# Optimization experiments

Hardware: AMD Instinct MI355X
Metric: run time of the kernel (lower is better)

## Reference

```python
import jax, jax.numpy as jnp
import numpy as np

N, F_IN, H, C, E = 50000, 512, 128, 64, 800000


def setup_inputs() -> dict:
    key = jax.random.key(0)
    ks = jax.random.split(key, 20)
    stdv = 1.0 / np.sqrt(H)
    std_att = 1.0
    std_att_vec = 1.0 / np.sqrt(3.0)
    u = lambda k, shape, s: jax.random.uniform(k, shape, jnp.float32, -s, s)
    inp = {
        "x": jax.random.normal(ks[0], (N, F_IN), jnp.float32),
        "edge_row": jax.random.randint(ks[1], (E,), 0, N, jnp.int32),
        "edge_col": jax.random.randint(ks[2], (E,), 0, N, jnp.int32),
        "edge_val": jax.random.uniform(ks[3], (E,), jnp.float32) * (1.0 / 16.0),
        "weight_low": u(ks[4], (F_IN, H), stdv),
        "weight_high": u(ks[5], (F_IN, H), stdv),
        "weight_mlp": u(ks[6], (F_IN, H), stdv),
        "att_vec_low": u(ks[7], (H, 1), std_att),
        "att_vec_high": u(ks[8], (H, 1), std_att),
        "att_vec_mlp": u(ks[9], (H, 1), std_att),
        "att_vec": u(ks[10], (3, 3), std_att_vec),
        "weight_low2": u(ks[11], (H, C), stdv),
        "weight_high2": u(ks[12], (H, C), stdv),
        "weight_mlp2": u(ks[13], (H, C), stdv),
        "att_vec_low2": u(ks[14], (C, 1), std_att),
        "att_vec_high2": u(ks[15], (C, 1), std_att),
        "att_vec_mlp2": u(ks[16], (C, 1), std_att),
        "att_vec2": u(ks[17], (3, 3), std_att_vec),
    }
    return inp


def _spmm_low(row, col, val, X):
    # adj_low @ X via gather + segment-sum over edges
    return jax.ops.segment_sum(val[:, None] * X[col], row, num_segments=N)


def _attention(o_low, o_high, o_mlp, a_low, a_high, a_mlp, a_vec):
    T = 3.0
    feats = jnp.concatenate([o_low @ a_low, o_high @ a_high, o_mlp @ a_mlp], axis=1)  # [N,3]
    att = jax.nn.softmax(jax.nn.sigmoid(feats) @ a_vec / T, axis=1)
    return att[:, 0:1], att[:, 1:2], att[:, 2:3]


def _layer(X, row, col, val, W_l, W_h, W_m, a_l, a_h, a_m, a_vec):
    xl = X @ W_l
    xh = X @ W_h
    o_low = jax.nn.relu(_spmm_low(row, col, val, xl))
    o_high = jax.nn.relu(xh - _spmm_low(row, col, val, xh))  # (I - adj_low) @ xh
    o_mlp = jax.nn.relu(X @ W_m)
    al, ah, am = _attention(o_low, o_high, o_mlp, a_l, a_h, a_m, a_vec)
    return 3.0 * (al * o_low + ah * o_high + am * o_mlp)


def reference(x, edge_row, edge_col, edge_val, weight_low, weight_high, weight_mlp,
              att_vec_low, att_vec_high, att_vec_mlp, att_vec,
              weight_low2, weight_high2, weight_mlp2,
              att_vec_low2, att_vec_high2, att_vec_mlp2, att_vec2):
    h = _layer(x, edge_row, edge_col, edge_val, weight_low, weight_high, weight_mlp,
               att_vec_low, att_vec_high, att_vec_mlp, att_vec)
    out = _layer(h, edge_row, edge_col, edge_val, weight_low2, weight_high2, weight_mlp2,
                 att_vec_low2, att_vec_high2, att_vec_mlp2, att_vec2)
    return jax.nn.log_softmax(out, axis=1)
```

## Files before the change

kernel.cpp:

```cpp
#include <hip/hip_runtime.h>
#include <hip/hip_bf16.h>

#define NN 50000
#define F_IN 512
#define HH 128
#define CC 64

typedef __attribute__((ext_vector_type(8))) short short8v;
typedef __attribute__((ext_vector_type(4))) float f32x4;
typedef __attribute__((ext_vector_type(2))) float f32x2;

__device__ __forceinline__ short f2b(float f) {
    unsigned u = __builtin_bit_cast(unsigned, f);
    unsigned r = (u + 0x7fffu + ((u >> 16) & 1u)) >> 16;
    return (short)r;
}
__device__ __forceinline__ float b2f(short s) {
    unsigned u = ((unsigned)(unsigned short)s) << 16;
    return __builtin_bit_cast(float, u);
}
__device__ __forceinline__ float b2f_lo(unsigned p) {
    return __builtin_bit_cast(float, p << 16);
}
__device__ __forceinline__ float b2f_hi(unsigned p) {
    return __builtin_bit_cast(float, p & 0xffff0000u);
}

__device__ __forceinline__ f32x2 q2_lo(unsigned p) {
    return __builtin_amdgcn_cvt_pk_f32_fp8(p, false);
}
__device__ __forceinline__ f32x2 q2_hi(unsigned p) {
    return __builtin_amdgcn_cvt_pk_f32_fp8(p, true);
}

__device__ __forceinline__ int xcd_swz(int bid, int nwg) {
    int q = nwg >> 3, r = nwg & 7;
    int xcd = bid & 7, off = bid >> 3;
    return (xcd < r ? xcd * (q + 1) : r * (q + 1) + (xcd - r) * q) + off;
}

__device__ __forceinline__ void load_lds16(const short* g, short* l) {
    __builtin_amdgcn_global_load_lds(
        (const __attribute__((address_space(1))) unsigned int*)g,
        (__attribute__((address_space(3))) unsigned int*)l,
        16, 0, 0);
}

template <int K, int OUTW>
__device__ __forceinline__ void wprep_body(const float* __restrict__ W0,
                                           const float* __restrict__ W1,
                                           const float* __restrict__ W2,
                                           short* __restrict__ Bt, int id) {
    const int nth = 3 * OUTW * (K / 8);
    if (id >= nth) return;
    const int n = id / (K / 8);
    const int kq = id % (K / 8);
    constexpr int HB = OUTW / 2;
    const int t = n / OUTW;
    const int r = n % OUTW;
    int sel, c;
    if (t < 2) { sel = (r >= HB) ? 1 : 0; c = t * HB + (r % HB); }
    else       { sel = 2; c = r; }
    const float* W = sel == 0 ? W0 : (sel == 1 ? W1 : W2);
    short v[8];
#pragma unroll
    for (int j = 0; j < 8; ++j) v[j] = f2b(W[(size_t)(kq * 8 + j) * OUTW + c]);
#pragma unroll
    for (int j = 0; j < 8; ++j) Bt[(size_t)n * K + kq * 8 + j] = v[j];
}

__global__ __launch_bounds__(256) void prep0(int* __restrict__ counts, int n,
                                             const float* __restrict__ Wl,
                                             const float* __restrict__ Wh,
                                             const float* __restrict__ Wm,
                                             short* __restrict__ Bt1,
                                             const float* __restrict__ Wl2,
                                             const float* __restrict__ Wh2,
                                             const float* __restrict__ Wm2,
                                             short* __restrict__ Bt2,
                                             int nZero, int nW1) {
    const int b = blockIdx.x;
    if (b < nZero) {
        int i = b * 256 + threadIdx.x;
        if (i < n) counts[i] = 0;
    } else if (b < nZero + nW1) {
        wprep_body<F_IN, HH>(Wl, Wh, Wm, Bt1, (b - nZero) * 256 + threadIdx.x);
    } else {
        wprep_body<HH, CC>(Wl2, Wh2, Wm2, Bt2, (b - nZero - nW1) * 256 + threadIdx.x);
    }
}

__global__ __launch_bounds__(256) void hist_xconv(const int* __restrict__ erow,
                                                  int* __restrict__ counts, int E,
                                                  const float* __restrict__ x,
                                                  short* __restrict__ xb, int n8,
                                                  int nHist) {
    const int b = blockIdx.x;
    const int total = gridDim.x;
    const long hb4 = ((long)b * nHist) / total;
    const long ha4 = ((long)(b + 1) * nHist) / total;
    if (ha4 != hb4) {
        int i = (int)hb4 * 256 + threadIdx.x;
        if (i < E) atomicAdd(&counts[erow[i]], 1);
        return;
    }
    int i = (b - (int)hb4) * 256 + threadIdx.x;
    if (i >= n8) return;
    const float4* xp = (const float4*)x;
    const float4 a = xp[2 * i];
    const float4 bb = xp[2 * i + 1];
    short8v o;
    o[0] = f2b(a.x); o[1] = f2b(a.y); o[2] = f2b(a.z); o[3] = f2b(a.w);
    o[4] = f2b(bb.x); o[5] = f2b(bb.y); o[6] = f2b(bb.z); o[7] = f2b(bb.w);
    *reinterpret_cast<short8v*>(&xb[(size_t)i * 8]) = o;
}

template <int K, int BNout>
__device__ __forceinline__ void gemm_body(const short* __restrict__ A,
                                          const short* __restrict__ Bt,
                                          unsigned* __restrict__ xq,
                                          short* __restrict__ xh,
                                          short* __restrict__ xm,
                                          int M, int wg, short* smem) {
    constexpr int BM = 128, BK = 64;
    constexpr int FM = (BNout == 128) ? 4 : 2;
    constexpr int FN = 4;
    constexpr int WM = FM * 16;
    constexpr int NKT = K / BK;
    constexpr int NBL = BNout / 32;
    constexpr int HB = BNout / 2;

    short* As = smem;
    short* Bs = smem + BM * BK;

    const int tid = threadIdx.x;
    const int lane = tid & 63;
    const int wid = tid >> 6;
    const int bm = wg / 3;
    const int bn = wg % 3;
    const int m0 = bm * BM;
    const int n0 = bn * BNout;
    const int wm = (BNout == 128) ? (wid >> 1) : wid;
    const int wn = (BNout == 128) ? (wid & 1) : 0;

    const int r8 = lane >> 3;
    const int sl = (lane & 7) ^ r8;

    f32x4 acc[FM][FN];
#pragma unroll
    for (int i = 0; i < FM; ++i)
#pragma unroll
        for (int j = 0; j < FN; ++j) acc[i][j] = (f32x4){0.f, 0.f, 0.f, 0.f};

    for (int kt = 0; kt < NKT; ++kt) {
        const int k0 = kt * BK;
        __syncthreads();
#pragma unroll
        for (int i = 0; i < 4; ++i) {
            int r = (wid * 4 + i) * 8 + r8;
            int gr = m0 + r; if (gr >= M) gr = M - 1;
            load_lds16(&A[(size_t)gr * K + k0 + sl * 8], &As[(wid * 4 + i) * 512]);
        }
#pragma unroll
        for (int i = 0; i < NBL; ++i) {
            int r = (wid * NBL + i) * 8 + r8;
            load_lds16(&Bt[(size_t)(n0 + r) * K + k0 + sl * 8],
                       &Bs[(wid * NBL + i) * 512]);
        }
        __syncthreads();

        const int mrow = lane & 15;
        const int kg = lane >> 4;
#pragma unroll
        for (int kk = 0; kk < 2; ++kk) {
            short8v af[FM], bf[FN];
#pragma unroll
            for (int f = 0; f < FM; ++f) {
                int m = wm * WM + f * 16 + mrow;
                int s = kk * 4 + kg;
                af[f] = *reinterpret_cast<const short8v*>(
                    &As[m * 64 + ((s ^ (m & 7)) << 3)]);
            }
#pragma unroll
            for (int f = 0; f < FN; ++f) {
                int nr = wn * 64 + f * 16 + mrow;
                int s = kk * 4 + kg;
                bf[f] = *reinterpret_cast<const short8v*>(
                    &Bs[nr * 64 + ((s ^ (nr & 7)) << 3)]);
            }
#pragma unroll
            for (int i = 0; i < FM; ++i)
#pragma unroll
                for (int j = 0; j < FN; ++j)
                    acc[i][j] = __builtin_amdgcn_mfma_f32_16x16x32_bf16(
                        af[i], bf[j], acc[i][j], 0, 0, 0);
        }
    }

    __syncthreads();
#pragma unroll
    for (int i = 0; i < FM; ++i)
#pragma unroll
        for (int j = 0; j < FN; ++j) {
            int cc = wn * 64 + j * 16 + (lane & 15);
#pragma unroll
            for (int e = 0; e < 4; ++e) {
                int r = wm * WM + i * 16 + (lane >> 4) * 4 + e;
                smem[r * BNout + cc] = f2b(acc[i][j][e]);
            }
        }
    __syncthreads();

    if (bn == 2) {
        constexpr int CH = BM * BNout / 8;
#pragma unroll
        for (int p = 0; p < CH / 256; ++p) {
            int idx = p * 256 + tid;
            int r = idx / (BNout / 8);
            int c8 = idx % (BNout / 8);
            int grow = m0 + r;
            if (grow < M)
                *reinterpret_cast<int4*>(&xm[(size_t)grow * BNout + c8 * 8]) =
                    *reinterpret_cast<const int4*>(&smem[r * BNout + c8 * 8]);
        }
    } else {
#pragma unroll
        for (int p = 0; p < (BM * (HB / 8)) / 256; ++p) {
            int idx = p * 256 + tid;
            int r = idx / (HB / 8);
            int c8 = idx % (HB / 8);
            int grow = m0 + r;
            if (grow < M)
                *reinterpret_cast<int4*>(&xh[(size_t)grow * BNout + bn * HB + c8 * 8]) =
                    *reinterpret_cast<const int4*>(&smem[r * BNout + HB + c8 * 8]);
        }
#pragma unroll
        for (int p = 0; p < (BM * (BNout / 4)) / 256; ++p) {
            int idx = p * 256 + tid;
            int r = idx / (BNout / 4);
            int k = idx % (BNout / 4);
            int grow = m0 + r;
            if (grow < M) {
                unsigned lw = *reinterpret_cast<const unsigned*>(&smem[r * BNout + 2 * k]);
                unsigned hw = *reinterpret_cast<const unsigned*>(&smem[r * BNout + HB + 2 * k]);
                unsigned w;
                if (BNout == 128) {
                    w = __builtin_amdgcn_cvt_pk_fp8_f32(b2f_lo(lw), b2f_hi(lw), 0, false);
                    w = __builtin_amdgcn_cvt_pk_fp8_f32(b2f_lo(hw), b2f_hi(hw), w, true);
                } else {
                    w = __builtin_amdgcn_cvt_pk_fp8_f32(b2f_lo(lw), b2f_lo(hw), 0, false);
                    w = __builtin_amdgcn_cvt_pk_fp8_f32(b2f_hi(lw), b2f_hi(hw), w, true);
                }
                xq[(size_t)grow * (BNout / 2) + bn * (BNout / 4) + k] = w;
            }
        }
    }
}

template <int K, int BNout>
__global__ __launch_bounds__(256) void gemm_scatter(const short* __restrict__ A,
                                                    const short* __restrict__ Bt,
                                                    unsigned* __restrict__ xq,
                                                    short* __restrict__ xh,
                                                    short* __restrict__ xm,
                                                    int M, int nGemm,
                                                    const int* __restrict__ row,
                                                    const int* __restrict__ col,
                                                    const float* __restrict__ val,
                                                    int* __restrict__ cursor,
                                                    int2* __restrict__ edges, int E,
                                                    int nScat) {
    __shared__ short smem[128 * 64 + BNout * 64];

    const int total = nGemm + nScat;
    const int swz = xcd_swz(blockIdx.x, total);
    const long ns_b = ((long)swz * nScat) / total;
    const long ns_a = ((long)(swz + 1) * nScat) / total;

    if (ns_a != ns_b) {
        int i = (int)ns_b * 256 + threadIdx.x;
        if (i < E) {
            int r = row[i];
            int p = atomicAdd(&cursor[r], 1);
            int2 rec;
            rec.x = col[i];
            rec.y = __builtin_bit_cast(int, val[i]);
            edges[p] = rec;
        }
        return;
    }
    gemm_body<K, BNout>(A, Bt, xq, xh, xm, M, swz - (int)ns_b, smem);
}

template <int K, int BNout>
__global__ __launch_bounds__(256) void gemm_mfma(const short* __restrict__ A,
                                                 const short* __restrict__ Bt,
                                                 unsigned* __restrict__ xq,
                                                 short* __restrict__ xh,
                                                 short* __restrict__ xm,
                                                 int M) {
    __shared__ short smem[128 * 64 + BNout * 64];
    gemm_body<K, BNout>(A, Bt, xq, xh, xm, M, xcd_swz(blockIdx.x, gridDim.x), smem);
}

__global__ __launch_bounds__(256) void block_sums_kernel(const int* __restrict__ counts,
                                                         int* __restrict__ bsums, int n) {
    __shared__ int s[256];
    int tid = threadIdx.x;
    int i = blockIdx.x * 256 + tid;
    s[tid] = (i < n) ? counts[i] : 0;
    __syncthreads();
#pragma unroll
    for (int off = 128; off > 0; off >>= 1) {
        if (tid < off) s[tid] += s[tid + off];
        __syncthreads();
    }
    if (tid == 0) bsums[blockIdx.x] = s[0];
}

__global__ __launch_bounds__(256) void scan_bsums_kernel(int* __restrict__ bsums, int nb) {
    __shared__ int s[256];
    int t = threadIdx.x;
    int v = (t < nb) ? bsums[t] : 0;
    s[t] = v;
    __syncthreads();
#pragma unroll
    for (int off = 1; off < 256; off <<= 1) {
        int u = (t >= off) ? s[t - off] : 0;
        __syncthreads();
        s[t] += u;
        __syncthreads();
    }
    if (t < nb) bsums[t] = s[t] - v;
}

__global__ __launch_bounds__(256) void scan_final_kernel(const int* __restrict__ counts,
                                                         const int* __restrict__ bsums,
                                                         int* __restrict__ rowptr,
                                                         int* __restrict__ cursor, int n) {
    __shared__ int s[256];
    int tid = threadIdx.x;
    int i = blockIdx.x * 256 + tid;
    int v = (i < n) ? counts[i] : 0;
    s[tid] = v;
    __syncthreads();
#pragma unroll
    for (int off = 1; off < 256; off <<= 1) {
        int t = (tid >= off) ? s[tid - off] : 0;
        __syncthreads();
        s[tid] += t;
        __syncthreads();
    }
    int excl = s[tid] - v + bsums[blockIdx.x];
    if (i < n) {
        rowptr[i] = excl;
        cursor[i] = excl;
        if (i == n - 1) rowptr[n] = excl + v;
    }
}

__device__ __forceinline__ float wave_sum(float v) {
#pragma unroll
    for (int off = 32; off > 0; off >>= 1) v += __shfl_xor(v, off, 64);
    return v;
}
__device__ __forceinline__ float wave_max(float v) {
#pragma unroll
    for (int off = 32; off > 0; off >>= 1) v = fmaxf(v, __shfl_xor(v, off, 64));
    return v;
}

__global__ __launch_bounds__(256) void spmm_att1(const int* __restrict__ rowptr,
                                                 const int2* __restrict__ edges,
                                                 const unsigned* __restrict__ xq,
                                                 const unsigned* __restrict__ xhp,
                                                 const unsigned* __restrict__ xmp,
                                                 const float* __restrict__ a_low,
                                                 const float* __restrict__ a_high,
                                                 const float* __restrict__ a_mlp,
                                                 const float* __restrict__ av,
                                                 short* __restrict__ hb,
                                                 int n) {
    const int node = blockIdx.x * 4 + (threadIdx.x >> 6);
    const int lane = threadIdx.x & 63;
    if (node >= n) return;

    const int s = __builtin_amdgcn_readfirstlane(rowptr[node]);
    const int e = __builtin_amdgcn_readfirstlane(rowptr[node + 1]);

    float l0 = 0.f, l1 = 0.f, h0 = 0.f, h1 = 0.f;
    for (int j = s; j < e; j += 8) {
        int   cq[8];
        float vq[8];
#pragma unroll
        for (int q = 0; q < 8; ++q) {
            const int jj = min(j + q, e - 1);
            const int2 rec = edges[jj];
            cq[q] = __builtin_amdgcn_readfirstlane(rec.x);
            int vb = __builtin_amdgcn_readfirstlane(rec.y);
            float t = __builtin_bit_cast(float, vb);
            vq[q] = (j + q < e) ? t : 0.f;
        }
        unsigned p[8];
#pragma unroll
        for (int q = 0; q < 8; ++q)
            p[q] = xq[(size_t)cq[q] * 64 + lane];
#pragma unroll
        for (int q = 0; q < 8; ++q) {
            const f32x2 lo = q2_lo(p[q]);
            const f32x2 hi = q2_hi(p[q]);
            l0 += vq[q] * lo.x; l1 += vq[q] * lo.y;
            h0 += vq[q] * hi.x; h1 += vq[q] * hi.y;
        }
    }

    const unsigned xhn = xhp[(size_t)node * 64 + lane];
    const unsigned xmn = xmp[(size_t)node * 64 + lane];
    float ol0 = fmaxf(l0, 0.f);
    float ol1 = fmaxf(l1, 0.f);
    float oh0 = fmaxf(b2f_lo(xhn) - h0, 0.f);
    float oh1 = fmaxf(b2f_hi(xhn) - h1, 0.f);
    float om0 = fmaxf(b2f_lo(xmn), 0.f);
    float om1 = fmaxf(b2f_hi(xmn), 0.f);

    const float2 aL = ((const float2*)a_low)[lane];
    const float2 aH = ((const float2*)a_high)[lane];
    const float2 aM = ((const float2*)a_mlp)[lane];
    float dl = wave_sum(ol0 * aL.x + ol1 * aL.y);
    float dh = wave_sum(oh0 * aH.x + oh1 * aH.y);
    float dm = wave_sum(om0 * aM.x + om1 * aM.y);

    const float g0 = 1.f / (1.f + expf(-dl));
    const float g1 = 1.f / (1.f + expf(-dh));
    const float g2 = 1.f / (1.f + expf(-dm));
    float s0 = (g0 * av[0] + g1 * av[3] + g2 * av[6]) * (1.f / 3.f);
    float s1 = (g0 * av[1] + g1 * av[4] + g2 * av[7]) * (1.f / 3.f);
    float s2 = (g0 * av[2] + g1 * av[5] + g2 * av[8]) * (1.f / 3.f);
    float mx = fmaxf(s0, fmaxf(s1, s2));
    float e0 = expf(s0 - mx), e1 = expf(s1 - mx), e2 = expf(s2 - mx);
    float inv = 1.f / (e0 + e1 + e2);
    float at0 = e0 * inv, at1 = e1 * inv, at2 = e2 * inv;

    float ho0 = 3.f * (at0 * ol0 + at1 * oh0 + at2 * om0);
    float ho1 = 3.f * (at0 * ol1 + at1 * oh1 + at2 * om1);
    unsigned pk = (unsigned)(unsigned short)f2b(ho0) |
                  ((unsigned)(unsigned short)f2b(ho1) << 16);
    ((unsigned*)hb)[(size_t)node * 64 + lane] = pk;
}

__global__ __launch_bounds__(256) void spmm_att2(const int* __restrict__ rowptr,
                                                 const int2* __restrict__ edges,
                                                 const unsigned short* __restrict__ xq,
                                                 const short* __restrict__ xhp,
                                                 const short* __restrict__ xmp,
                                                 const float* __restrict__ a_low,
                                                 const float* __restrict__ a_high,
                                                 const float* __restrict__ a_mlp,
                                                 const float* __restrict__ av,
                                                 float* __restrict__ out,
                                                 int n) {
    const int node = blockIdx.x * 4 + (threadIdx.x >> 6);
    const int lane = threadIdx.x & 63;
    if (node >= n) return;

    const int s = __builtin_amdgcn_readfirstlane(rowptr[node]);
    const int e = __builtin_amdgcn_readfirstlane(rowptr[node + 1]);

    float accl = 0.f, acch = 0.f;
    for (int j = s; j < e; j += 8) {
        int   cq[8];
        float vq[8];
#pragma unroll
        for (int q = 0; q < 8; ++q) {
            const int jj = min(j + q, e - 1);
            const int2 rec = edges[jj];
            cq[q] = __builtin_amdgcn_readfirstlane(rec.x);
            int vb = __builtin_amdgcn_readfirstlane(rec.y);
            float t = __builtin_bit_cast(float, vb);
            vq[q] = (j + q < e) ? t : 0.f;
        }
        unsigned short p[8];
#pragma unroll
        for (int q = 0; q < 8; ++q)
            p[q] = xq[(size_t)cq[q] * 64 + lane];
#pragma unroll
        for (int q = 0; q < 8; ++q) {
            const f32x2 d = q2_lo((unsigned)p[q]);
            accl += vq[q] * d.x;
            acch += vq[q] * d.y;
        }
    }

    float ol = fmaxf(accl, 0.f);
    float oh = fmaxf(b2f(xhp[(size_t)node * 64 + lane]) - acch, 0.f);
    float om = fmaxf(b2f(xmp[(size_t)node * 64 + lane]), 0.f);

    float dl = wave_sum(ol * a_low[lane]);
    float dh = wave_sum(oh * a_high[lane]);
    float dm = wave_sum(om * a_mlp[lane]);

    const float g0 = 1.f / (1.f + expf(-dl));
    const float g1 = 1.f / (1.f + expf(-dh));
    const float g2 = 1.f / (1.f + expf(-dm));
    float s0 = (g0 * av[0] + g1 * av[3] + g2 * av[6]) * (1.f / 3.f);
    float s1 = (g0 * av[1] + g1 * av[4] + g2 * av[7]) * (1.f / 3.f);
    float s2 = (g0 * av[2] + g1 * av[5] + g2 * av[8]) * (1.f / 3.f);
    float mx3 = fmaxf(s0, fmaxf(s1, s2));
    float e0 = expf(s0 - mx3), e1 = expf(s1 - mx3), e2 = expf(s2 - mx3);
    float inv = 1.f / (e0 + e1 + e2);
    float at0 = e0 * inv, at1 = e1 * inv, at2 = e2 * inv;

    float o = 3.f * (at0 * ol + at1 * oh + at2 * om);

    float m = wave_max(o);
    float ex = expf(o - m);
    float su = wave_sum(ex);
    out[(size_t)node * 64 + lane] = o - m - logf(su);
}

extern "C" void kernel_launch(void* const* d_in, const int* in_sizes, int n_in,
                              void* d_out, int out_size, void* d_ws, size_t ws_size,
                              hipStream_t stream) {
    const float* x    = (const float*)d_in[0];
    const int*   erow = (const int*)d_in[1];
    const int*   ecol = (const int*)d_in[2];
    const float* eval = (const float*)d_in[3];
    const float* Wl   = (const float*)d_in[4];
    const float* Wh   = (const float*)d_in[5];
    const float* Wm   = (const float*)d_in[6];
    const float* al   = (const float*)d_in[7];
    const float* ah   = (const float*)d_in[8];
    const float* am   = (const float*)d_in[9];
    const float* av   = (const float*)d_in[10];
    const float* Wl2  = (const float*)d_in[11];
    const float* Wh2  = (const float*)d_in[12];
    const float* Wm2  = (const float*)d_in[13];
    const float* al2  = (const float*)d_in[14];
    const float* ah2  = (const float*)d_in[15];
    const float* am2  = (const float*)d_in[16];
    const float* av2  = (const float*)d_in[17];
    float* out = (float*)d_out;

    const int E = in_sizes[1];
    const int N = NN;

    short* ws    = (short*)d_ws;
    short* xb    = ws;
    short* xh1   = xb + (size_t)N * 512;
    short* xm1   = xh1 + (size_t)N * 128;
    short* hb    = xm1 + (size_t)N * 128;
    unsigned* xq1 = (unsigned*)(hb + (size_t)N * 128);
    short* Bt1   = (short*)(xq1 + (size_t)N * 64);
    short* Bt2   = Bt1 + 384 * 512;
    int*   ip    = (int*)(Bt2 + 192 * 128);
    int*   counts = ip;
    int*   rowptr = ip + N;
    int*   cursor = ip + 2 * N + 1;
    int*   bsums  = ip + 3 * N + 1;
    int2*  edges  = (int2*)(((size_t)(ip + 3 * N + 1 + 256) + 15) & ~(size_t)15);

    unsigned* xq2 = xq1;
    short* xh2 = xh1;
    short* xm2 = xh1 + (size_t)N * 64;

    const int NB = (N + 255) / 256;
    const int EB = (E + 255) / 256;
    const int node_blocks = (N + 3) / 4;
    const int MT = (N + 127) / 128;
    const int XCB = (N * F_IN / 8 + 255) / 256;
    const int W1B = (3 * HH * (F_IN / 8) + 255) / 256;
    const int W2B = (3 * CC * (HH / 8) + 255) / 256;
    const int nGemm1 = MT * 3;

    prep0<<<NB + W1B + W2B, 256, 0, stream>>>(counts, N, Wl, Wh, Wm, Bt1,
                                              Wl2, Wh2, Wm2, Bt2, NB, W1B);
    hist_xconv<<<EB + XCB, 256, 0, stream>>>(erow, counts, E, x, xb,
                                             N * F_IN / 8, EB);
    block_sums_kernel<<<NB, 256, 0, stream>>>(counts, bsums, N);
    scan_bsums_kernel<<<1, 256, 0, stream>>>(bsums, NB);
    scan_final_kernel<<<NB, 256, 0, stream>>>(counts, bsums, rowptr, cursor, N);

    gemm_scatter<F_IN, HH><<<nGemm1 + EB, 256, 0, stream>>>(
        xb, Bt1, xq1, xh1, xm1, N, nGemm1, erow, ecol, eval, cursor, edges, E, EB);
    spmm_att1<<<node_blocks, 256, 0, stream>>>(rowptr, edges, xq1,
                                               (const unsigned*)xh1,
                                               (const unsigned*)xm1,
                                               al, ah, am, av, hb, N);

    gemm_mfma<HH, CC><<<MT * 3, 256, 0, stream>>>(hb, Bt2, xq2, xh2, xm2, N);
    spmm_att2<<<node_blocks, 256, 0, stream>>>(rowptr, edges,
                                               (const unsigned short*)xq2,
                                               xh2, xm2,
                                               al2, ah2, am2, av2, out, N);
}
```

Measured before the change: 195.9 us.

## Double-buffer GEMM LDS tiles with BK=32 and explicit vmcnt waits

```diff
diff --git a/kernel.cpp b/kernel.cpp
--- a/kernel.cpp
+++ b/kernel.cpp
@@ -122,16 +122,16 @@
                                           short* __restrict__ xh,
                                           short* __restrict__ xm,
                                           int M, int wg, short* smem) {
-    constexpr int BM = 128, BK = 64;
+    constexpr int BM = 128, BK = 32;
     constexpr int FM = (BNout == 128) ? 4 : 2;
     constexpr int FN = 4;
     constexpr int WM = FM * 16;
     constexpr int NKT = K / BK;
-    constexpr int NBL = BNout / 32;
+    constexpr int AW = (BM * BK / 512) / 4;
+    constexpr int BW_ = (BNout * BK / 512) / 4;
+    constexpr int VMC = AW + BW_;
+    constexpr int HALF = BM * BK + BNout * BK;
     constexpr int HB = BNout / 2;
-
-    short* As = smem;
-    short* Bs = smem + BM * BK;
 
     const int tid = threadIdx.x;
     const int lane = tid & 63;
@@ -143,8 +143,8 @@
     const int wm = (BNout == 128) ? (wid >> 1) : wid;
     const int wn = (BNout == 128) ? (wid & 1) : 0;
 
-    const int r8 = lane >> 3;
-    const int sl = (lane & 7) ^ r8;
+    const int rl = lane >> 2;
+    const int sl = (lane & 3) ^ ((lane >> 3) & 3);
 
     f32x4 acc[FM][FN];
 #pragma unroll
@@ -152,52 +152,67 @@
 #pragma unroll
         for (int j = 0; j < FN; ++j) acc[i][j] = (f32x4){0.f, 0.f, 0.f, 0.f};
 
+    auto issue = [&](int kt, int b) {
+        const int k0 = kt * BK;
+        short* As = smem + b * HALF;
+        short* Bs = As + BM * BK;
+#pragma unroll
+        for (int i = 0; i < AW; ++i) {
+            int g = wid * AW + i;
+            int r = g * 16 + rl;
+            int gr = m0 + r; if (gr >= M) gr = M - 1;
+            load_lds16(&A[(size_t)gr * K + k0 + sl * 8], &As[g * 512]);
+        }
+#pragma unroll
+        for (int i = 0; i < BW_; ++i) {
+            int g = wid * BW_ + i;
+            int r = g * 16 + rl;
+            load_lds16(&Bt[(size_t)(n0 + r) * K + k0 + sl * 8], &Bs[g * 512]);
+        }
+    };
+
+    issue(0, 0);
+
+    const int mrow = lane & 15;
+    const int kg = lane >> 4;
     for (int kt = 0; kt < NKT; ++kt) {
-        const int k0 = kt * BK;
-        __syncthreads();
-#pragma unroll
-        for (int i = 0; i < 4; ++i) {
-            int r = (wid * 4 + i) * 8 + r8;
-            int gr = m0 + r; if (gr >= M) gr = M - 1;
-            load_lds16(&A[(size_t)gr * K + k0 + sl * 8], &As[(wid * 4 + i) * 512]);
-        }
-#pragma unroll
-        for (int i = 0; i < NBL; ++i) {
-            int r = (wid * NBL + i) * 8 + r8;
-            load_lds16(&Bt[(size_t)(n0 + r) * K + k0 + sl * 8],
-                       &Bs[(wid * NBL + i) * 512]);
-        }
-        __syncthreads();
-
-        const int mrow = lane & 15;
-        const int kg = lane >> 4;
-#pragma unroll
-        for (int kk = 0; kk < 2; ++kk) {
-            short8v af[FM], bf[FN];
-#pragma unroll
-            for (int f = 0; f < FM; ++f) {
-                int m = wm * WM + f * 16 + mrow;
-                int s = kk * 4 + kg;
-                af[f] = *reinterpret_cast<const short8v*>(
-                    &As[m * 64 + ((s ^ (m & 7)) << 3)]);
-            }
-#pragma unroll
-            for (int f = 0; f < FN; ++f) {
-                int nr = wn * 64 + f * 16 + mrow;
-                int s = kk * 4 + kg;
-                bf[f] = *reinterpret_cast<const short8v*>(
-                    &Bs[nr * 64 + ((s ^ (nr & 7)) << 3)]);
-            }
-#pragma unroll
-            for (int i = 0; i < FM; ++i)
-#pragma unroll
-                for (int j = 0; j < FN; ++j)
-                    acc[i][j] = __builtin_amdgcn_mfma_f32_16x16x32_bf16(
-                        af[i], bf[j], acc[i][j], 0, 0, 0);
-        }
-    }
-
-    __syncthreads();
+        const int cur = kt & 1;
+        if (kt + 1 < NKT) {
+            issue(kt + 1, cur ^ 1);
+            asm volatile("s_waitcnt vmcnt(%0)" :: "n"(VMC) : "memory");
+        } else {
+            asm volatile("s_waitcnt vmcnt(0)" ::: "memory");
+        }
+        __builtin_amdgcn_s_barrier();
+        __builtin_amdgcn_sched_barrier(0);
+
+        const short* As = smem + cur * HALF;
+        const short* Bs = As + BM * BK;
+        short8v af[FM], bf[FN];
+#pragma unroll
+        for (int f = 0; f < FM; ++f) {
+            int m = wm * WM + f * 16 + mrow;
+            af[f] = *reinterpret_cast<const short8v*>(
+                &As[m * 32 + ((kg ^ ((m >> 1) & 3)) << 3)]);
+        }
+#pragma unroll
+        for (int f = 0; f < FN; ++f) {
+            int nr = wn * 64 + f * 16 + mrow;
+            bf[f] = *reinterpret_cast<const short8v*>(
+                &Bs[nr * 32 + ((kg ^ ((nr >> 1) & 3)) << 3)]);
+        }
+#pragma unroll
+        for (int i = 0; i < FM; ++i)
+#pragma unroll
+            for (int j = 0; j < FN; ++j)
+                acc[i][j] = __builtin_amdgcn_mfma_f32_16x16x32_bf16(
+                    af[i], bf[j], acc[i][j], 0, 0, 0);
+
+        asm volatile("s_waitcnt lgkmcnt(0)" ::: "memory");
+        __builtin_amdgcn_sched_barrier(0);
+        __builtin_amdgcn_s_barrier();
+    }
+
 #pragma unroll
     for (int i = 0; i < FM; ++i)
 #pragma unroll
@@ -257,6 +272,13 @@
     }
 }
 
+template <int BNout>
+struct GemmSmem {
+    static constexpr int SM1 = 2 * (128 * 32 + BNout * 32);
+    static constexpr int SM2 = 128 * BNout;
+    static constexpr int SZ = SM1 > SM2 ? SM1 : SM2;
+};
+
 template <int K, int BNout>
 __global__ __launch_bounds__(256) void gemm_scatter(const short* __restrict__ A,
                                                     const short* __restrict__ Bt,
@@ -270,7 +292,7 @@
                                                     int* __restrict__ cursor,
                                                     int2* __restrict__ edges, int E,
                                                     int nScat) {
-    __shared__ short smem[128 * 64 + BNout * 64];
+    __shared__ short smem[GemmSmem<BNout>::SZ];
 
     const int total = nGemm + nScat;
     const int swz = xcd_swz(blockIdx.x, total);
@@ -299,7 +321,7 @@
                                                  short* __restrict__ xh,
                                                  short* __restrict__ xm,
                                                  int M) {
-    __shared__ short smem[128 * 64 + BNout * 64];
+    __shared__ short smem[GemmSmem<BNout>::SZ];
     gemm_body<K, BNout>(A, Bt, xq, xh, xm, M, xcd_swz(blockIdx.x, gridDim.x), smem);
 }
 
```

Measured after the change: 195.1 us, median of 2. About the same (-0.4%).
